# Performance work log

Hardware: AMD Instinct MI355X
Metric: run time of the kernel (lower is better)

## Reference

```python
import jax, jax.numpy as jnp
import numpy as np

RES = 256      # cubic grid resolution
CH = 16        # feature channels
RR = 8         # reduced_res = ceil(log2(RES))
MASK = 128     # low-frequency mask size
N_PTS = 262144 # query points


def _bilinear(feat, gx, gy):
    """torch.F.grid_sample, bilinear, align_corners=True, zero padding.
    feat: (C,H,W); gx,gy: (N,) in [-1,1] (gx indexes W, gy indexes H).
    Returns (N,C)."""
    H, W = feat.shape[1], feat.shape[2]
    x = (gx + 1.0) * 0.5 * (W - 1)
    y = (gy + 1.0) * 0.5 * (H - 1)
    x0 = jnp.floor(x)
    y0 = jnp.floor(y)
    wx = x - x0
    wy = y - y0
    x0i = jnp.clip(x0.astype(jnp.int32), 0, W - 1)
    x1i = jnp.clip(x0i + 1, 0, W - 1)
    y0i = jnp.clip(y0.astype(jnp.int32), 0, H - 1)
    y1i = jnp.clip(y0i + 1, 0, H - 1)
    v00 = feat[:, y0i, x0i]
    v01 = feat[:, y0i, x1i]
    v10 = feat[:, y1i, x0i]
    v11 = feat[:, y1i, x1i]
    out = (v00 * (1 - wx) * (1 - wy) + v01 * wx * (1 - wy)
           + v10 * (1 - wx) * wy + v11 * wx * wy)  # (C,N)
    return out.T


def _plane(P, mask2d, gx, gy, icoord):
    """One phasor plane: mask -> ifft2 -> grid_sample -> Fourier integration.
    P: (CH*RR, RES, RES, 2); returns (N, CH)."""
    Pc = (P[..., 0] + 1j * P[..., 1]) * mask2d          # (C,H,W) complex
    Pc = jnp.fft.ifft2(Pc)                              # ifft over last 2 axes
    C = P.shape[0]
    # interleave (real, imag) per complex channel, like permute+reshape in torch
    feat = jnp.stack([Pc.real, Pc.imag], axis=1).reshape(2 * C, RES, RES)
    samp = _bilinear(feat, gx, gy).reshape(-1, 2 * CH, RR)  # (N, 2*CH, RR)
    Z = samp[:, :CH] + 1j * samp[:, CH:]                    # (N, CH, RR)
    s = (icoord + 1.0) * 0.5 * (2 ** RR - 1)                # scaled coord
    coef = 2.0 ** jnp.arange(RR) - 1.0                      # (RR,)
    basis = jnp.exp(2j * jnp.pi * s[:, None] * coef / (2 ** RR))  # (N, RR)
    return jnp.einsum('nr,ncr->nc', basis, Z).real


def _forward(Pu, Pv, Pw, inputs):
    mask2d = jnp.zeros((RES, RES), jnp.float32).at[:MASK, :MASK].set(1.0)
    out = (_plane(Pu, mask2d, inputs[:, 1], inputs[:, 2], inputs[:, 0])
           + _plane(Pv, mask2d, inputs[:, 0], inputs[:, 2], inputs[:, 1])
           + _plane(Pw, mask2d, inputs[:, 0], inputs[:, 1], inputs[:, 2]))
    return out  # (N, CH)


def setup_inputs() -> dict:
    key = jax.random.key(0)
    k1, k2, k3, k4 = jax.random.split(key, 4)
    Pu = 0.001 * jax.random.normal(k1, (CH * RR, RES, RES, 2), jnp.float32)
    Pv = 0.001 * jax.random.normal(k2, (CH * RR, RES, RES, 2), jnp.float32)
    Pw = 0.001 * jax.random.normal(k3, (CH * RR, RES, RES, 2), jnp.float32)
    inputs = jax.random.uniform(k4, (N_PTS, 3), jnp.float32, -1.0, 1.0)
    return {"Pu": Pu, "Pv": Pv, "Pw": Pw, "inputs": inputs}


def reference(Pu, Pv, Pw, inputs):
    return _forward(Pu, Pv, Pw, inputs)
```

## Files before the change

### kernel.cpp

```cpp
#include <hip/hip_runtime.h>
#include <hip/hip_bf16.h>
#include <cmath>


#define NPTS 262144

__device__ __forceinline__ int brev8(int x) { return (int)(__brev((unsigned)x) >> 24); }

__device__ __forceinline__ unsigned pack_bf16(float2 v) {
    unsigned short a = __builtin_bit_cast(unsigned short, __float2bfloat16(v.x));
    unsigned short b = __builtin_bit_cast(unsigned short, __float2bfloat16(v.y));
    return (unsigned)a | ((unsigned)b << 16);
}
__device__ __forceinline__ float2 unpack_bf16(unsigned u) {
    return make_float2(__uint_as_float(u << 16), __uint_as_float(u & 0xffff0000u));
}

__device__ __forceinline__ void plane_coords(int p, float in0, float in1, float in2,
                                             float& gx, float& gy, float& sc) {
    gx = (p == 0) ? in1 : in0;
    gy = (p == 2) ? in1 : in2;
    sc = (p == 0) ? in0 : ((p == 1) ? in1 : in2);
}

__global__ __launch_bounds__(512) void pass1_kernel(const float* __restrict__ P0,
                                                    const float* __restrict__ P1,
                                                    const float* __restrict__ P2,
                                                    unsigned* __restrict__ X) {
    __shared__ float2 tw[128];
    __shared__ float2 tile[256 * 17];

    int t = threadIdx.x;
    if (t < 128) {
        float s, c;
        sincospif((float)t * (1.0f / 128.0f), &s, &c);
        tw[t] = make_float2(c, s);
    }
    int plane = blockIdx.y;
    const float* P = (plane == 0) ? P0 : ((plane == 1) ? P1 : P2);
    unsigned* Xp = X + (size_t)plane * 4194304;

    int b  = blockIdx.x;
    int ch = b >> 3;
    int x0 = (b & 7) << 4;
    const float* src = P + (size_t)ch * 131072 + x0 * 2;

    const float scale = 1.0f / 65536.0f;
#pragma unroll
    for (int k = 0; k < 2; k++) {
        int i = t + (k << 9);
        int y = i >> 3;
        int j = i & 7;
        float4 v = *(const float4*)(src + (size_t)y * 512 + (j << 2));
        float2 c0 = make_float2(v.x * scale, v.y * scale);
        float2 c1 = make_float2(v.z * scale, v.w * scale);
        int pos = brev8(y);
        tile[pos * 17 + 2 * j]           = c0;
        tile[(pos + 1) * 17 + 2 * j]     = c0;
        tile[pos * 17 + 2 * j + 1]       = c1;
        tile[(pos + 1) * 17 + 2 * j + 1] = c1;
    }
    __syncthreads();
#pragma unroll
    for (int s = 2; s <= 8; s++) {
        int half = 1 << (s - 1);
        int col = t & 15;
        int bb  = t >> 4;
#pragma unroll
        for (int k = 0; k < 4; k++) {
            int bf = bb + (k << 5);
            int j  = bf & (half - 1);
            int g  = bf >> (s - 1);
            int i0 = (g << s) + j;
            int i1 = i0 + half;
            float2 u = tile[i0 * 17 + col];
            float2 v = tile[i1 * 17 + col];
            float2 w = tw[j << (8 - s)];
            float2 vt = make_float2(v.x * w.x - v.y * w.y, v.x * w.y + v.y * w.x);
            tile[i0 * 17 + col] = make_float2(u.x + vt.x, u.y + vt.y);
            tile[i1 * 17 + col] = make_float2(u.x - vt.x, u.y - vt.y);
        }
        __syncthreads();
    }
    unsigned* dst = Xp + (size_t)ch * 32768 + x0;
#pragma unroll
    for (int k = 0; k < 8; k++) {
        int i = t + (k << 9);
        int v = i >> 4;
        int col = i & 15;
        dst[(size_t)v * 128 + col] = pack_bf16(tile[v * 17 + col]);
    }
}

__global__ __launch_bounds__(1024) void pass2_kernel(const unsigned* __restrict__ X,
                                                     __hip_bfloat16* __restrict__ feat) {
    __shared__ float2 tw[128];
    __shared__ float2 rows[16 * 257];

    int t = threadIdx.x;
    if (t < 128) {
        float s, c;
        sincospif((float)t * (1.0f / 128.0f), &s, &c);
        tw[t] = make_float2(c, s);
    }
    int w = t >> 6;
    int l = t & 63;
    int v   = blockIdx.x & 255;
    int g   = blockIdx.x >> 8;
    int ch0 = g << 4;
    int ch  = ch0 + w;
    int plane = blockIdx.y;
    const unsigned* Xp = X + (size_t)plane * 4194304;
    __hip_bfloat16* fp = feat + (size_t)plane * 16777216;

    const uint2* src = (const uint2*)(Xp + ((size_t)ch * 256 + v) * 128);
    uint2 d = src[l];
    float2 c0 = unpack_bf16(d.x);
    float2 c1 = unpack_bf16(d.y);
    float2* row = rows + w * 257;
    int p0 = brev8(2 * l);
    int p1 = brev8(2 * l + 1);
    row[p0]     = c0;
    row[p0 + 1] = c0;
    row[p1]     = c1;
    row[p1 + 1] = c1;
    __syncthreads();
#pragma unroll
    for (int s = 2; s <= 8; s++) {
        int half = 1 << (s - 1);
#pragma unroll
        for (int k = 0; k < 2; k++) {
            int bf = l + (k << 6);
            int j  = bf & (half - 1);
            int gg = bf >> (s - 1);
            int i0 = (gg << s) + j;
            int i1 = i0 + half;
            float2 u  = row[i0];
            float2 vv = row[i1];
            float2 wq = tw[j << (8 - s)];
            float2 vt = make_float2(vv.x * wq.x - vv.y * wq.y,
                                    vv.x * wq.y + vv.y * wq.x);
            row[i0] = make_float2(u.x + vt.x, u.y + vt.y);
            row[i1] = make_float2(u.x - vt.x, u.y - vt.y);
        }
        __syncthreads();
    }
    __hip_bfloat16* dst = fp + (size_t)v * 65536 + (ch0 << 1);
#pragma unroll
    for (int k = 0; k < 8; k++) {
        int f = t + (k << 10);
        int x = f >> 5;
        int j = f & 31;
        float2 cpx = rows[(j >> 1) * 257 + x];
        float val = (j & 1) ? cpx.y : cpx.x;
        dst[x * 256 + j] = __float2bfloat16(val);
    }
}

__device__ __forceinline__ int tile_key(int p, float in0, float in1, float in2) {
    float gx, gy, sc;
    plane_coords(p, in0, in1, in2, gx, gy, sc);
    float xf = (gx + 1.0f) * 127.5f;
    float yf = (gy + 1.0f) * 127.5f;
    int x0 = max(0, min((int)floorf(xf), 255));
    int y0 = max(0, min((int)floorf(yf), 255));
    return (y0 & 0xF0) | (x0 >> 4);
}

__global__ __launch_bounds__(1024) void hist_kernel(const float* __restrict__ pts,
                                                    unsigned* __restrict__ hist) {
    __shared__ unsigned hb[256];
    int t = threadIdx.x;
    int p = blockIdx.y;
    int n = (blockIdx.x << 10) + t;
    if (t < 256) hb[t] = 0;
    __syncthreads();
    float in0 = pts[3 * n + 0], in1 = pts[3 * n + 1], in2 = pts[3 * n + 2];
    int key = tile_key(p, in0, in1, in2);
    atomicAdd(&hb[key], 1u);
    __syncthreads();
    if (t < 256 && hb[t]) atomicAdd(&hist[(p << 8) + t], hb[t]);
}

__global__ __launch_bounds__(256) void scan_kernel(const unsigned* __restrict__ hist,
                                                   unsigned* __restrict__ cursor) {
    __shared__ unsigned s[256];
    int t = threadIdx.x;
    for (int p = 0; p < 3; p++) {
        unsigned v = hist[(p << 8) + t];
        s[t] = v;
        __syncthreads();
#pragma unroll
        for (int d = 1; d < 256; d <<= 1) {
            unsigned add = (t >= d) ? s[t - d] : 0u;
            __syncthreads();
            s[t] += add;
            __syncthreads();
        }
        cursor[(p << 8) + t] = s[t] - v;
        __syncthreads();
    }
}

__global__ __launch_bounds__(1024) void scatter_kernel(const float* __restrict__ pts,
                                                       unsigned* __restrict__ cursor,
                                                       int* __restrict__ order) {
    __shared__ unsigned cnt[256];
    __shared__ unsigned base[256];
    int t = threadIdx.x;
    int p = blockIdx.y;
    int n = (blockIdx.x << 10) + t;
    if (t < 256) cnt[t] = 0;
    __syncthreads();
    float in0 = pts[3 * n + 0], in1 = pts[3 * n + 1], in2 = pts[3 * n + 2];
    int key = tile_key(p, in0, in1, in2);
    unsigned rank = atomicAdd(&cnt[key], 1u);
    __syncthreads();
    if (t < 256 && cnt[t]) base[t] = atomicAdd(&cursor[(p << 8) + t], cnt[t]);
    __syncthreads();
    order[p * NPTS + base[key] + rank] = n;
}

__device__ __forceinline__ float dot8(uint4 d, const float* wr) {
    float a0 = __uint_as_float(d.x << 16);
    float a1 = __uint_as_float(d.x & 0xffff0000u);
    float a2 = __uint_as_float(d.y << 16);
    float a3 = __uint_as_float(d.y & 0xffff0000u);
    float a4 = __uint_as_float(d.z << 16);
    float a5 = __uint_as_float(d.z & 0xffff0000u);
    float a6 = __uint_as_float(d.w << 16);
    float a7 = __uint_as_float(d.w & 0xffff0000u);
    return wr[0] * a0 + wr[1] * a1 + wr[2] * a2 + wr[3] * a3 +
           wr[4] * a4 + wr[5] * a5 + wr[6] * a6 + wr[7] * a7;
}

__global__ __launch_bounds__(256) void gather_kernel(const ushort* __restrict__ feat,
                                                     const int* __restrict__ order,
                                                     const float* __restrict__ pts,
                                                     float* __restrict__ partial) {
    int t = threadIdx.x;
    int w = t >> 6;
    int l = t & 63;
    int h = l >> 5;
    int q = l & 31;
    int p = blockIdx.y;
    const ushort* fb = feat + (size_t)p * 16777216;

    int idx = (blockIdx.x << 3) + (w << 1) + h;
    int n = order[p * NPTS + idx];
    float in0 = pts[3 * n + 0], in1 = pts[3 * n + 1], in2 = pts[3 * n + 2];
    float gx, gy, sc;
    plane_coords(p, in0, in1, in2, gx, gy, sc);

    float xf = (gx + 1.0f) * 127.5f;
    float yf = (gy + 1.0f) * 127.5f;
    float x0f = floorf(xf);
    float y0f = floorf(yf);
    float wx = xf - x0f;
    float wy = yf - y0f;
    int x0 = max(0, min((int)x0f, 255));
    int y0 = max(0, min((int)y0f, 255));
    int x1 = min(x0 + 1, 255);
    int y1 = min(y0 + 1, 255);

    uint4 d00 = *((const uint4*)(fb + (((y0 << 8) + x0) << 8)) + q);
    uint4 d01 = *((const uint4*)(fb + (((y0 << 8) + x1) << 8)) + q);
    uint4 d10 = *((const uint4*)(fb + (((y1 << 8) + x0) << 8)) + q);
    uint4 d11 = *((const uint4*)(fb + (((y1 << 8) + x1) << 8)) + q);

    float coef = (float)((1 << (q & 7)) - 1);
    float a = (sc + 1.0f) * 0.99609375f * coef;
    float sn, cs;
    sincospif(a, &sn, &cs);
    float merged = (q < 16) ? cs : -sn;
    float wr[8];
#pragma unroll
    for (int i = 0; i < 8; i++) wr[i] = __shfl(merged, (l & 48) + i);

    float s00 = dot8(d00, wr);
    float s01 = dot8(d01, wr);
    float s10 = dot8(d10, wr);
    float s11 = dot8(d11, wr);

    float w00 = (1.0f - wx) * (1.0f - wy);
    float w01 = wx * (1.0f - wy);
    float w10 = (1.0f - wx) * wy;
    float w11 = wx * wy;
    float acc = w00 * s00 + w01 * s01 + w10 * s10 + w11 * s11;

    acc += __shfl_xor(acc, 16);
    if (q < 16) {
        partial[(((size_t)p * NPTS + n) << 4) + q] = acc;
    }
}

__global__ __launch_bounds__(256) void combine_kernel(const float4* __restrict__ pa,
                                                      float4* __restrict__ out) {
    int i = (blockIdx.x << 8) + threadIdx.x;
    float4 a = pa[i];
    float4 b = pa[i + 1048576];
    float4 c = pa[i + 2097152];
    out[i] = make_float4(a.x + b.x + c.x, a.y + b.y + c.y,
                         a.z + b.z + c.z, a.w + b.w + c.w);
}

extern "C" void kernel_launch(void* const* d_in, const int* in_sizes, int n_in,
                              void* d_out, int out_size, void* d_ws, size_t ws_size,
                              hipStream_t stream) {
    const float* P0  = (const float*)d_in[0];
    const float* P1  = (const float*)d_in[1];
    const float* P2  = (const float*)d_in[2];
    const float* pts = (const float*)d_in[3];
    float* out = (float*)d_out;
    char* ws = (char*)d_ws;

    __hip_bfloat16* feat = (__hip_bfloat16*)ws;
    unsigned* X          = (unsigned*)(ws + 100663296u);
    float*    partial    = (float*)(ws + 150994944u);
    int*      order      = (int*)(ws + 201326592u);
    unsigned* hist       = (unsigned*)(ws + 204472320u);
    unsigned* cursor     = (unsigned*)(ws + 204475392u);

    hipMemsetAsync(hist, 0, 3072, stream);

    dim3 g1(1024, 3);
    pass1_kernel<<<g1, 512, 0, stream>>>(P0, P1, P2, X);
    dim3 g2(2048, 3);
    pass2_kernel<<<g2, 1024, 0, stream>>>(X, feat);

    dim3 gs(256, 3);
    hist_kernel<<<gs, 1024, 0, stream>>>(pts, hist);
    scan_kernel<<<1, 256, 0, stream>>>(hist, cursor);
    scatter_kernel<<<gs, 1024, 0, stream>>>(pts, cursor, order);

    dim3 gg(32768, 3);
    gather_kernel<<<gg, 256, 0, stream>>>((const ushort*)feat, order, pts, partial);
    combine_kernel<<<4096, 256, 0, stream>>>((const float4*)partial, (float4*)out);
}
```

Baseline: 416.3 us.

## Sort pre-computed point records, drop FFT barriers, pack bilinear math in gather

The scatter kernel now writes sorted float4 records (gx, gy, sc, index), so the gather no longer does an indirect read of the points and recomputes plane coordinates. In pass1, columns are remapped so each wave owns its own FFT columns. That lets the per-stage __syncthreads move out of the butterfly loops in both FFT passes, relying on in-order LDS access within a wave. The gather also swizzles its block order, derives neighbour addresses from one base pointer, and does the bilinear-then-basis reduction with packed two-wide float math. In exchange, the sorted buffer takes four times the memory traffic of the old index array.

```diff
diff --git a/kernel.cpp b/kernel.cpp
--- a/kernel.cpp
+++ b/kernel.cpp
@@ -4,6 +4,8 @@
 
 
 #define NPTS 262144
+
+typedef float vf2 __attribute__((ext_vector_type(2)));
 
 __device__ __forceinline__ int brev8(int x) { return (int)(__brev((unsigned)x) >> 24); }
 
@@ -14,6 +16,10 @@
 }
 __device__ __forceinline__ float2 unpack_bf16(unsigned u) {
     return make_float2(__uint_as_float(u << 16), __uint_as_float(u & 0xffff0000u));
+}
+__device__ __forceinline__ vf2 up2(unsigned u) {
+    vf2 r; r.x = __uint_as_float(u << 16); r.y = __uint_as_float(u & 0xffff0000u);
+    return r;
 }
 
 __device__ __forceinline__ void plane_coords(int p, float in0, float in1, float in2,
@@ -61,11 +67,13 @@
         tile[(pos + 1) * 17 + 2 * j + 1] = c1;
     }
     __syncthreads();
+
+    int w = t >> 6, l = t & 63;
+    int col = (w << 1) + (l & 1);
+    int bb  = l >> 1;
 #pragma unroll
     for (int s = 2; s <= 8; s++) {
         int half = 1 << (s - 1);
-        int col = t & 15;
-        int bb  = t >> 4;
 #pragma unroll
         for (int k = 0; k < 4; k++) {
             int bf = bb + (k << 5);
@@ -75,20 +83,21 @@
             int i1 = i0 + half;
             float2 u = tile[i0 * 17 + col];
             float2 v = tile[i1 * 17 + col];
-            float2 w = tw[j << (8 - s)];
-            float2 vt = make_float2(v.x * w.x - v.y * w.y, v.x * w.y + v.y * w.x);
+            float2 wq = tw[j << (8 - s)];
+            float2 vt = make_float2(v.x * wq.x - v.y * wq.y, v.x * wq.y + v.y * wq.x);
             tile[i0 * 17 + col] = make_float2(u.x + vt.x, u.y + vt.y);
             tile[i1 * 17 + col] = make_float2(u.x - vt.x, u.y - vt.y);
         }
-        __syncthreads();
-    }
+    }
+    __syncthreads();
+
     unsigned* dst = Xp + (size_t)ch * 32768 + x0;
 #pragma unroll
     for (int k = 0; k < 8; k++) {
         int i = t + (k << 9);
         int v = i >> 4;
-        int col = i & 15;
-        dst[(size_t)v * 128 + col] = pack_bf16(tile[v * 17 + col]);
+        int c = i & 15;
+        dst[(size_t)v * 128 + c] = pack_bf16(tile[v * 17 + c]);
     }
 }
 
@@ -143,8 +152,8 @@
             row[i0] = make_float2(u.x + vt.x, u.y + vt.y);
             row[i1] = make_float2(u.x - vt.x, u.y - vt.y);
         }
-        __syncthreads();
-    }
+    }
+    __syncthreads();
     __hip_bfloat16* dst = fp + (size_t)v * 65536 + (ch0 << 1);
 #pragma unroll
     for (int k = 0; k < 8; k++) {
@@ -157,9 +166,7 @@
     }
 }
 
-__device__ __forceinline__ int tile_key(int p, float in0, float in1, float in2) {
-    float gx, gy, sc;
-    plane_coords(p, in0, in1, in2, gx, gy, sc);
+__device__ __forceinline__ int tile_key(float gx, float gy) {
     float xf = (gx + 1.0f) * 127.5f;
     float yf = (gy + 1.0f) * 127.5f;
     int x0 = max(0, min((int)floorf(xf), 255));
@@ -176,8 +183,9 @@
     if (t < 256) hb[t] = 0;
     __syncthreads();
     float in0 = pts[3 * n + 0], in1 = pts[3 * n + 1], in2 = pts[3 * n + 2];
-    int key = tile_key(p, in0, in1, in2);
-    atomicAdd(&hb[key], 1u);
+    float gx, gy, sc;
+    plane_coords(p, in0, in1, in2, gx, gy, sc);
+    atomicAdd(&hb[tile_key(gx, gy)], 1u);
     __syncthreads();
     if (t < 256 && hb[t]) atomicAdd(&hist[(p << 8) + t], hb[t]);
 }
@@ -204,7 +212,7 @@
 
 __global__ __launch_bounds__(1024) void scatter_kernel(const float* __restrict__ pts,
                                                        unsigned* __restrict__ cursor,
-                                                       int* __restrict__ order) {
+                                                       float4* __restrict__ psort) {
     __shared__ unsigned cnt[256];
     __shared__ unsigned base[256];
     int t = threadIdx.x;
@@ -213,30 +221,18 @@
     if (t < 256) cnt[t] = 0;
     __syncthreads();
     float in0 = pts[3 * n + 0], in1 = pts[3 * n + 1], in2 = pts[3 * n + 2];
-    int key = tile_key(p, in0, in1, in2);
+    float gx, gy, sc;
+    plane_coords(p, in0, in1, in2, gx, gy, sc);
+    int key = tile_key(gx, gy);
     unsigned rank = atomicAdd(&cnt[key], 1u);
     __syncthreads();
     if (t < 256 && cnt[t]) base[t] = atomicAdd(&cursor[(p << 8) + t], cnt[t]);
     __syncthreads();
-    order[p * NPTS + base[key] + rank] = n;
-}
-
-__device__ __forceinline__ float dot8(uint4 d, const float* wr) {
-    float a0 = __uint_as_float(d.x << 16);
-    float a1 = __uint_as_float(d.x & 0xffff0000u);
-    float a2 = __uint_as_float(d.y << 16);
-    float a3 = __uint_as_float(d.y & 0xffff0000u);
-    float a4 = __uint_as_float(d.z << 16);
-    float a5 = __uint_as_float(d.z & 0xffff0000u);
-    float a6 = __uint_as_float(d.w << 16);
-    float a7 = __uint_as_float(d.w & 0xffff0000u);
-    return wr[0] * a0 + wr[1] * a1 + wr[2] * a2 + wr[3] * a3 +
-           wr[4] * a4 + wr[5] * a5 + wr[6] * a6 + wr[7] * a7;
+    psort[p * NPTS + base[key] + rank] = make_float4(gx, gy, sc, __int_as_float(n));
 }
 
 __global__ __launch_bounds__(256) void gather_kernel(const ushort* __restrict__ feat,
-                                                     const int* __restrict__ order,
-                                                     const float* __restrict__ pts,
+                                                     const float4* __restrict__ psort,
                                                      float* __restrict__ partial) {
     int t = threadIdx.x;
     int w = t >> 6;
@@ -246,11 +242,12 @@
     int p = blockIdx.y;
     const ushort* fb = feat + (size_t)p * 16777216;
 
-    int idx = (blockIdx.x << 3) + (w << 1) + h;
-    int n = order[p * NPTS + idx];
-    float in0 = pts[3 * n + 0], in1 = pts[3 * n + 1], in2 = pts[3 * n + 2];
-    float gx, gy, sc;
-    plane_coords(p, in0, in1, in2, gx, gy, sc);
+    int b  = blockIdx.x;
+    int lb = ((b & 7) << 12) | (b >> 3);
+    int idx = (lb << 3) + (w << 1) + h;
+    float4 pt = psort[p * NPTS + idx];
+    float gx = pt.x, gy = pt.y, sc = pt.z;
+    int n = __float_as_int(pt.w);
 
     float xf = (gx + 1.0f) * 127.5f;
     float yf = (gy + 1.0f) * 127.5f;
@@ -260,33 +257,45 @@
     float wy = yf - y0f;
     int x0 = max(0, min((int)x0f, 255));
     int y0 = max(0, min((int)y0f, 255));
-    int x1 = min(x0 + 1, 255);
-    int y1 = min(y0 + 1, 255);
-
-    uint4 d00 = *((const uint4*)(fb + (((y0 << 8) + x0) << 8)) + q);
-    uint4 d01 = *((const uint4*)(fb + (((y0 << 8) + x1) << 8)) + q);
-    uint4 d10 = *((const uint4*)(fb + (((y1 << 8) + x0) << 8)) + q);
-    uint4 d11 = *((const uint4*)(fb + (((y1 << 8) + x1) << 8)) + q);
+    int dx = (x0 < 255) ? 256 : 0;
+    int dy = (y0 < 255) ? 65536 : 0;
+
+    const ushort* bp = fb + (((y0 << 8) + x0) << 8) + (q << 3);
+    uint4 d00 = *(const uint4*)bp;
+    uint4 d01 = *(const uint4*)(bp + dx);
+    uint4 d10 = *(const uint4*)(bp + dy);
+    uint4 d11 = *(const uint4*)(bp + dx + dy);
 
     float coef = (float)((1 << (q & 7)) - 1);
     float a = (sc + 1.0f) * 0.99609375f * coef;
     float sn, cs;
     sincospif(a, &sn, &cs);
     float merged = (q < 16) ? cs : -sn;
-    float wr[8];
-#pragma unroll
-    for (int i = 0; i < 8; i++) wr[i] = __shfl(merged, (l & 48) + i);
-
-    float s00 = dot8(d00, wr);
-    float s01 = dot8(d01, wr);
-    float s10 = dot8(d10, wr);
-    float s11 = dot8(d11, wr);
+    float wr0 = __shfl(merged, (l & 48) + 0);
+    float wr1 = __shfl(merged, (l & 48) + 1);
+    float wr2 = __shfl(merged, (l & 48) + 2);
+    float wr3 = __shfl(merged, (l & 48) + 3);
+    float wr4 = __shfl(merged, (l & 48) + 4);
+    float wr5 = __shfl(merged, (l & 48) + 5);
+    float wr6 = __shfl(merged, (l & 48) + 6);
+    float wr7 = __shfl(merged, (l & 48) + 7);
 
     float w00 = (1.0f - wx) * (1.0f - wy);
     float w01 = wx * (1.0f - wy);
     float w10 = (1.0f - wx) * wy;
     float w11 = wx * wy;
-    float acc = w00 * s00 + w01 * s01 + w10 * s10 + w11 * s11;
+
+    vf2 b0 = w00 * up2(d00.x) + w01 * up2(d01.x) + w10 * up2(d10.x) + w11 * up2(d11.x);
+    vf2 b1 = w00 * up2(d00.y) + w01 * up2(d01.y) + w10 * up2(d10.y) + w11 * up2(d11.y);
+    vf2 b2 = w00 * up2(d00.z) + w01 * up2(d01.z) + w10 * up2(d10.z) + w11 * up2(d11.z);
+    vf2 b3 = w00 * up2(d00.w) + w01 * up2(d01.w) + w10 * up2(d10.w) + w11 * up2(d11.w);
+
+    vf2 wa; wa.x = wr0; wa.y = wr1;
+    vf2 wb; wb.x = wr2; wb.y = wr3;
+    vf2 wc; wc.x = wr4; wc.y = wr5;
+    vf2 wd; wd.x = wr6; wd.y = wr7;
+    vf2 acc2 = b0 * wa + b1 * wb + b2 * wc + b3 * wd;
+    float acc = acc2.x + acc2.y;
 
     acc += __shfl_xor(acc, 16);
     if (q < 16) {
@@ -317,9 +326,9 @@
     __hip_bfloat16* feat = (__hip_bfloat16*)ws;
     unsigned* X          = (unsigned*)(ws + 100663296u);
     float*    partial    = (float*)(ws + 150994944u);
-    int*      order      = (int*)(ws + 201326592u);
-    unsigned* hist       = (unsigned*)(ws + 204472320u);
-    unsigned* cursor     = (unsigned*)(ws + 204475392u);
+    float4*   psort      = (float4*)(ws + 201326592u);
+    unsigned* hist       = (unsigned*)(ws + 213909504u);
+    unsigned* cursor     = (unsigned*)(ws + 213912576u);
 
     hipMemsetAsync(hist, 0, 3072, stream);
 
@@ -331,9 +340,9 @@
     dim3 gs(256, 3);
     hist_kernel<<<gs, 1024, 0, stream>>>(pts, hist);
     scan_kernel<<<1, 256, 0, stream>>>(hist, cursor);
-    scatter_kernel<<<gs, 1024, 0, stream>>>(pts, cursor, order);
+    scatter_kernel<<<gs, 1024, 0, stream>>>(pts, cursor, psort);
 
     dim3 gg(32768, 3);
-    gather_kernel<<<gg, 256, 0, stream>>>((const ushort*)feat, order, pts, partial);
+    gather_kernel<<<gg, 256, 0, stream>>>((const ushort*)feat, psort, partial);
     combine_kernel<<<4096, 256, 0, stream>>>((const float4*)partial, (float4*)out);
 }
```

New measurement: 395.7 us. -4.9%, faster.
